# Optimization experiments

Measured on AMD Instinct MI355X. Metric: run time of the kernel, lower is better.

## Reference

```python
import jax, jax.numpy as jnp
import numpy as np

EPS = 1e-5  # torch LayerNorm default


def haar_dwt2(x):
    # pywt.dwt2(x, 'haar') on last two axes.
    # For each 2x2 block [[a,b],[c,d]]:
    #   LL=(a+b+c+d)/2, LH=(a+b-c-d)/2 (detail along rows),
    #   HL=(a-b+c-d)/2 (detail along cols), HH=(a-b-c+d)/2
    B, C, H, W = x.shape
    xb = x.reshape(B, C, H // 2, 2, W // 2, 2)
    a = xb[:, :, :, 0, :, 0]
    b = xb[:, :, :, 0, :, 1]
    c = xb[:, :, :, 1, :, 0]
    d = xb[:, :, :, 1, :, 1]
    ll = (a + b + c + d) * 0.5
    lh = (a + b - c - d) * 0.5
    hl = (a - b + c - d) * 0.5
    hh = (a - b - c + d) * 0.5
    return jnp.concatenate([ll, lh, hl, hh], axis=1)  # [B, 4C, H/2, W/2]


def setup_inputs() -> dict:
    key = jax.random.key(0)
    k1, k2 = jax.random.split(key)
    B, C, H, W = 16, 96, 256, 256
    x = jax.random.normal(k1, (B, C, H, W), dtype=jnp.float32)
    norm_w = jnp.ones((4 * C,), dtype=jnp.float32)
    norm_b = jnp.zeros((4 * C,), dtype=jnp.float32)
    w_red = jax.random.normal(k2, (4 * C, 2 * C), dtype=jnp.float32) * (1.0 / np.sqrt(4 * C))
    return {"x": x, "norm_w": norm_w, "norm_b": norm_b, "w_red": w_red}


def reference(x, norm_w, norm_b, w_red):
    B, C, H, W = x.shape
    y = haar_dwt2(x)                               # [B, 4C, H/2, W/2]
    y = y.reshape(B, 4 * C, -1).transpose(0, 2, 1)  # [B, L, 4C]
    mu = jnp.mean(y, axis=-1, keepdims=True)
    var = jnp.mean(jnp.square(y - mu), axis=-1, keepdims=True)
    y = (y - mu) * jax.lax.rsqrt(var + EPS) * norm_w + norm_b
    out = jnp.einsum('blc,cd->bld', y, w_red)       # [B, L, 2C]
    return out
```

## Files before the change

### kernel.cpp

```cpp
#include <hip/hip_runtime.h>
#include <hip/hip_bf16.h>

typedef __attribute__((ext_vector_type(8))) short short8;
typedef __attribute__((ext_vector_type(4))) float floatx4;

static __device__ __forceinline__ unsigned f2bf(float f) {
    unsigned u = __builtin_bit_cast(unsigned, f);
    unsigned r = u + 0x7fffu + ((u >> 16) & 1u);
    return r >> 16;
}
static __device__ __forceinline__ unsigned pk2bf(float lo, float hi) {
    return f2bf(lo) | (f2bf(hi) << 16);
}

__global__ __launch_bounds__(384)
void prep_kernel(const float* __restrict__ nw,
                 const float* __restrict__ nb,
                 const float* __restrict__ W,
                 __hip_bfloat16* __restrict__ Tt,
                 float* __restrict__ uvec,
                 float* __restrict__ vvec)
{
    __shared__ float su[384];
    __shared__ float sv[384];
    const int d = blockIdx.x;
    const int t = threadIdx.x;

    const int c  = t >> 2;
    const int rr = (t >> 1) & 1;
    const int q  = t & 1;

    float w0 = W[(0 * 96 + c) * 192 + d];
    float w1 = W[(1 * 96 + c) * 192 + d];
    float w2 = W[(2 * 96 + c) * 192 + d];
    float w3 = W[(3 * 96 + c) * 192 + d];
    float n0 = nw[0 * 96 + c];
    float n1 = nw[1 * 96 + c];
    float n2 = nw[2 * 96 + c];
    float n3 = nw[3 * 96 + c];

    float slh = rr ? -1.f : 1.f;
    float shl = q  ? -1.f : 1.f;
    float shh = (rr ^ q) ? -1.f : 1.f;
    float tv = 0.5f * (n0 * w0 + slh * n1 * w1 + shl * n2 * w2 + shh * n3 * w3);
    ((unsigned short*)Tt)[d * 384 + t] = (unsigned short)f2bf(tv);

    float wt = W[t * 192 + d];
    su[t] = nw[t] * wt;
    sv[t] = nb[t] * wt;
    __syncthreads();
    if (t < 64) {
        float a = su[t] + su[t + 64] + su[t + 128] + su[t + 192] + su[t + 256] + su[t + 320];
        float b = sv[t] + sv[t + 64] + sv[t + 128] + sv[t + 192] + sv[t + 256] + sv[t + 320];
        for (int off = 32; off; off >>= 1) {
            a += __shfl_down(a, off);
            b += __shfl_down(b, off);
        }
        if (t == 0) { uvec[d] = a; vvec[d] = b; }
    }
}

__global__ __launch_bounds__(256, 2)
void fused_kernel(const float* __restrict__ x,
                  const __hip_bfloat16* __restrict__ Tt,
                  const float* __restrict__ uvec,
                  const float* __restrict__ vvec,
                  float* __restrict__ out)
{
    constexpr int PK = 392;
    __shared__ __align__(16) __hip_bfloat16 As[64 * PK];
    __shared__ float S1p[256];
    __shared__ float S2p[256];
    __shared__ float2 ab[64];

    const int t  = threadIdx.x;
    const int bi = blockIdx.x;
    const int mb = bi & 1;
    const int h  = (bi >> 1) & 127;
    const int b  = bi >> 8;

    {
        const int m  = t & 63;
        const int cg = t >> 6;
        const float2* xrow =
            (const float2*)(x + ((size_t)b * 96 * 65536 + (size_t)(2 * h) * 256))
            + (mb * 64 + m);
        float s1 = 0.f, s2 = 0.f;
#pragma unroll
        for (int i = 0; i < 24; ++i) {
            const int ch = cg * 24 + i;
            const float2* p = xrow + (size_t)ch * 32768;
            float2 tp = p[0];
            float2 bt = p[128];
            s1 += tp.x;
            s2 += tp.x * tp.x + tp.y * tp.y + bt.x * bt.x + bt.y * bt.y;
            *(uint2*)(&As[m * PK + ch * 4]) =
                make_uint2(pk2bf(tp.x, tp.y), pk2bf(bt.x, bt.y));
        }
        S1p[t] = s1;
        S2p[t] = s2;
    }
    __syncthreads();
    if (t < 64) {
        float S1 = S1p[t] + S1p[t + 64] + S1p[t + 128] + S1p[t + 192];
        float S2 = S2p[t] + S2p[t + 64] + S2p[t + 128] + S2p[t + 192];
        float mu  = S1 * (2.0f / 384.0f);
        float var = S2 * (1.0f / 384.0f) - mu * mu;
        float rs  = rsqrtf(var + 1e-5f);
        ab[t] = make_float2(rs, -rs * mu);
    }
    __syncthreads();

    const int lane = t & 63;
    const int wv   = t >> 6;
    const int l15  = lane & 15;
    const int q2   = lane >> 4;

    const short8* Ap0 = (const short8*)(Tt + (size_t)(wv * 48 + l15) * 384 + q2 * 8);
    const short8* Bp0 = (const short8*)(&As[l15 * PK + q2 * 8]);

    floatx4 acc[3][4];
#pragma unroll
    for (int dt = 0; dt < 3; ++dt)
#pragma unroll
        for (int p = 0; p < 4; ++p)
            acc[dt][p] = (floatx4){0.f, 0.f, 0.f, 0.f};

#pragma unroll 2
    for (int ks = 0; ks < 12; ++ks) {
        short8 af[3], bf[4];
#pragma unroll
        for (int dt = 0; dt < 3; ++dt) af[dt] = Ap0[dt * 768 + ks * 4];
#pragma unroll
        for (int p = 0; p < 4; ++p) bf[p] = Bp0[p * 784 + ks * 4];
#pragma unroll
        for (int dt = 0; dt < 3; ++dt)
#pragma unroll
            for (int p = 0; p < 4; ++p)
                acc[dt][p] = __builtin_amdgcn_mfma_f32_16x16x32_bf16(
                    af[dt], bf[p], acc[dt][p], 0, 0, 0);
    }

    float2 abv[4];
#pragma unroll
    for (int p = 0; p < 4; ++p) abv[p] = ab[p * 16 + l15];

    const size_t outbase = ((size_t)b * 16384 + (size_t)h * 128 + mb * 64) * 192;
#pragma unroll
    for (int dt = 0; dt < 3; ++dt) {
        const int drow = wv * 48 + dt * 16 + q2 * 4;
        floatx4 uu = *(const floatx4*)(uvec + drow);
        floatx4 vv = *(const floatx4*)(vvec + drow);
#pragma unroll
        for (int p = 0; p < 4; ++p) {
            const int pos = p * 16 + l15;
            const float al = abv[p].x, be = abv[p].y;
            floatx4 o;
            o[0] = al * acc[dt][p][0] + be * uu[0] + vv[0];
            o[1] = al * acc[dt][p][1] + be * uu[1] + vv[1];
            o[2] = al * acc[dt][p][2] + be * uu[2] + vv[2];
            o[3] = al * acc[dt][p][3] + be * uu[3] + vv[3];
            *(floatx4*)(out + outbase + (size_t)pos * 192 + drow) = o;
        }
    }
}

extern "C" void kernel_launch(void* const* d_in, const int* in_sizes, int n_in,
                              void* d_out, int out_size, void* d_ws, size_t ws_size,
                              hipStream_t stream)
{
    const float* x  = (const float*)d_in[0];
    const float* nw = (const float*)d_in[1];
    const float* nb = (const float*)d_in[2];
    const float* W  = (const float*)d_in[3];
    float* out = (float*)d_out;

    __hip_bfloat16* Tt = (__hip_bfloat16*)d_ws;
    float* uvec = (float*)((char*)d_ws + 384 * 192 * 2);
    float* vvec = uvec + 192;

    prep_kernel<<<192, 384, 0, stream>>>(nw, nb, W, Tt, uvec, vvec);
    fused_kernel<<<4096, 256, 0, stream>>>(x, Tt, uvec, vvec, out);
}
```

Measured before the change: 634.5 us.

## Vectorize x loads with nontemporal float4, prefetch weights, raise occupancy

The load phase now reads x as 16-byte nontemporal vectors, with each thread covering two output positions across 12 channels instead of float2 loads over 24 channels. Partial sums are combined with a cross-lane shuffle before a smaller shared reduction. The first two k-steps of the weight tile and the u/v vectors are loaded before the x phase so their latency overlaps it. The bf16 packing uses the hardware cvt_pk instruction, and launch bounds ask for 3 blocks per CU. The risks are register pressure under the higher occupancy target and a different LDS store pattern that may cause bank conflicts.

```diff
diff --git a/kernel.cpp b/kernel.cpp
--- a/kernel.cpp
+++ b/kernel.cpp
@@ -10,7 +10,12 @@
     return r >> 16;
 }
 static __device__ __forceinline__ unsigned pk2bf(float lo, float hi) {
-    return f2bf(lo) | (f2bf(hi) << 16);
+    unsigned r;
+    asm("v_cvt_pk_bf16_f32 %0, %1, %2" : "=v"(r) : "v"(lo), "v"(hi));
+    return r;
+}
+static __device__ __forceinline__ floatx4 ntload(const floatx4* p) {
+    return __builtin_nontemporal_load(p);
 }
 
 __global__ __launch_bounds__(384)
@@ -60,7 +65,7 @@
     }
 }
 
-__global__ __launch_bounds__(256, 2)
+__global__ __launch_bounds__(256, 3)
 void fused_kernel(const float* __restrict__ x,
                   const __hip_bfloat16* __restrict__ Tt,
                   const float* __restrict__ uvec,
@@ -69,9 +74,7 @@
 {
     constexpr int PK = 392;
     __shared__ __align__(16) __hip_bfloat16 As[64 * PK];
-    __shared__ float S1p[256];
-    __shared__ float S2p[256];
-    __shared__ float2 ab[64];
+    __shared__ __align__(16) float S12[4][32][4];
 
     const int t  = threadIdx.x;
     const int bi = blockIdx.x;
@@ -79,44 +82,76 @@
     const int h  = (bi >> 1) & 127;
     const int b  = bi >> 8;
 
-    {
-        const int m  = t & 63;
-        const int cg = t >> 6;
-        const float2* xrow =
-            (const float2*)(x + ((size_t)b * 96 * 65536 + (size_t)(2 * h) * 256))
-            + (mb * 64 + m);
-        float s1 = 0.f, s2 = 0.f;
-#pragma unroll
-        for (int i = 0; i < 24; ++i) {
-            const int ch = cg * 24 + i;
-            const float2* p = xrow + (size_t)ch * 32768;
-            float2 tp = p[0];
-            float2 bt = p[128];
-            s1 += tp.x;
-            s2 += tp.x * tp.x + tp.y * tp.y + bt.x * bt.x + bt.y * bt.y;
-            *(uint2*)(&As[m * PK + ch * 4]) =
-                make_uint2(pk2bf(tp.x, tp.y), pk2bf(bt.x, bt.y));
-        }
-        S1p[t] = s1;
-        S2p[t] = s2;
-    }
-    __syncthreads();
-    if (t < 64) {
-        float S1 = S1p[t] + S1p[t + 64] + S1p[t + 128] + S1p[t + 192];
-        float S2 = S2p[t] + S2p[t + 64] + S2p[t + 128] + S2p[t + 192];
-        float mu  = S1 * (2.0f / 384.0f);
-        float var = S2 * (1.0f / 384.0f) - mu * mu;
-        float rs  = rsqrtf(var + 1e-5f);
-        ab[t] = make_float2(rs, -rs * mu);
-    }
-    __syncthreads();
-
     const int lane = t & 63;
     const int wv   = t >> 6;
     const int l15  = lane & 15;
     const int q2   = lane >> 4;
 
     const short8* Ap0 = (const short8*)(Tt + (size_t)(wv * 48 + l15) * 384 + q2 * 8);
+    short8 a0_0 = Ap0[0 * 768 + 0];
+    short8 a0_1 = Ap0[1 * 768 + 0];
+    short8 a0_2 = Ap0[2 * 768 + 0];
+    short8 a1_0 = Ap0[0 * 768 + 4];
+    short8 a1_1 = Ap0[1 * 768 + 4];
+    short8 a1_2 = Ap0[2 * 768 + 4];
+
+    {
+        const int f  = t & 31;
+        const int cg = t >> 5;
+        const floatx4* xt =
+            (const floatx4*)(x + ((size_t)b * 96 + cg) * 65536 + (size_t)(2 * h) * 256)
+            + (mb * 32 + f);
+        float s1a = 0.f, s2a = 0.f, s1b = 0.f, s2b = 0.f;
+#pragma unroll
+        for (int i = 0; i < 12; ++i) {
+            const floatx4* p = xt + (size_t)i * 131072;
+            floatx4 v = ntload(p);
+            floatx4 u = ntload(p + 64);
+            s1a += v[0];
+            s1b += v[2];
+            s2a += v[0] * v[0] + v[1] * v[1] + u[0] * u[0] + u[1] * u[1];
+            s2b += v[2] * v[2] + v[3] * v[3] + u[2] * u[2] + u[3] * u[3];
+            const int col = (cg + 8 * i) * 4;
+            *(uint2*)(&As[(2 * f) * PK + col]) =
+                make_uint2(pk2bf(v[0], v[1]), pk2bf(u[0], u[1]));
+            *(uint2*)(&As[(2 * f + 1) * PK + col]) =
+                make_uint2(pk2bf(v[2], v[3]), pk2bf(u[2], u[3]));
+        }
+        float r1a = s1a + __shfl_xor(s1a, 32);
+        float r2a = s2a + __shfl_xor(s2a, 32);
+        float r1b = s1b + __shfl_xor(s1b, 32);
+        float r2b = s2b + __shfl_xor(s2b, 32);
+        if (lane < 32) {
+            *(floatx4*)&S12[wv][f][0] = (floatx4){r1a, r2a, r1b, r2b};
+        }
+    }
+    __syncthreads();
+
+    if (t < 64) {
+        floatx4 r = *(const floatx4*)&S12[0][t >> 1][0];
+        r += *(const floatx4*)&S12[1][t >> 1][0];
+        r += *(const floatx4*)&S12[2][t >> 1][0];
+        r += *(const floatx4*)&S12[3][t >> 1][0];
+        float S1 = (t & 1) ? r[2] : r[0];
+        float S2 = (t & 1) ? r[3] : r[1];
+        float mu  = S1 * (2.0f / 384.0f);
+        float var = S2 * (1.0f / 384.0f) - mu * mu;
+        float rs  = rsqrtf(var + 1e-5f);
+        ((float2*)S12)[t] = make_float2(rs, -rs * mu);
+    }
+    __syncthreads();
+
+    const int dbase = wv * 48 + q2 * 4;
+    floatx4 uu[3], vv[3];
+#pragma unroll
+    for (int dt = 0; dt < 3; ++dt) {
+        uu[dt] = *(const floatx4*)(uvec + dbase + dt * 16);
+        vv[dt] = *(const floatx4*)(vvec + dbase + dt * 16);
+    }
+    float2 abv[4];
+#pragma unroll
+    for (int p = 0; p < 4; ++p) abv[p] = ((const float2*)S12)[p * 16 + l15];
+
     const short8* Bp0 = (const short8*)(&As[l15 * PK + q2 * 8]);
 
     floatx4 acc[3][4];
@@ -126,40 +161,55 @@
         for (int p = 0; p < 4; ++p)
             acc[dt][p] = (floatx4){0.f, 0.f, 0.f, 0.f};
 
-#pragma unroll 2
-    for (int ks = 0; ks < 12; ++ks) {
-        short8 af[3], bf[4];
-#pragma unroll
-        for (int dt = 0; dt < 3; ++dt) af[dt] = Ap0[dt * 768 + ks * 4];
-#pragma unroll
-        for (int p = 0; p < 4; ++p) bf[p] = Bp0[p * 784 + ks * 4];
+    {
+        short8 af[3] = {a0_0, a0_1, a0_2};
+        short8 bf[4];
+#pragma unroll
+        for (int p = 0; p < 4; ++p) bf[p] = Bp0[p * 784 + 0];
 #pragma unroll
         for (int dt = 0; dt < 3; ++dt)
 #pragma unroll
             for (int p = 0; p < 4; ++p)
                 acc[dt][p] = __builtin_amdgcn_mfma_f32_16x16x32_bf16(
                     af[dt], bf[p], acc[dt][p], 0, 0, 0);
-    }
-
-    float2 abv[4];
-#pragma unroll
-    for (int p = 0; p < 4; ++p) abv[p] = ab[p * 16 + l15];
+        short8 ag[3] = {a1_0, a1_1, a1_2};
+#pragma unroll
+        for (int p = 0; p < 4; ++p) bf[p] = Bp0[p * 784 + 4];
+#pragma unroll
+        for (int dt = 0; dt < 3; ++dt)
+#pragma unroll
+            for (int p = 0; p < 4; ++p)
+                acc[dt][p] = __builtin_amdgcn_mfma_f32_16x16x32_bf16(
+                    ag[dt], bf[p], acc[dt][p], 0, 0, 0);
+    }
+#pragma unroll 2
+    for (int ks = 2; ks < 12; ++ks) {
+        short8 af[3], bf[4];
+#pragma unroll
+        for (int dt = 0; dt < 3; ++dt) af[dt] = Ap0[dt * 768 + ks * 4];
+#pragma unroll
+        for (int p = 0; p < 4; ++p) bf[p] = Bp0[p * 784 + ks * 4];
+#pragma unroll
+        for (int dt = 0; dt < 3; ++dt)
+#pragma unroll
+            for (int p = 0; p < 4; ++p)
+                acc[dt][p] = __builtin_amdgcn_mfma_f32_16x16x32_bf16(
+                    af[dt], bf[p], acc[dt][p], 0, 0, 0);
+    }
 
     const size_t outbase = ((size_t)b * 16384 + (size_t)h * 128 + mb * 64) * 192;
 #pragma unroll
     for (int dt = 0; dt < 3; ++dt) {
         const int drow = wv * 48 + dt * 16 + q2 * 4;
-        floatx4 uu = *(const floatx4*)(uvec + drow);
-        floatx4 vv = *(const floatx4*)(vvec + drow);
 #pragma unroll
         for (int p = 0; p < 4; ++p) {
             const int pos = p * 16 + l15;
             const float al = abv[p].x, be = abv[p].y;
             floatx4 o;
-            o[0] = al * acc[dt][p][0] + be * uu[0] + vv[0];
-            o[1] = al * acc[dt][p][1] + be * uu[1] + vv[1];
-            o[2] = al * acc[dt][p][2] + be * uu[2] + vv[2];
-            o[3] = al * acc[dt][p][3] + be * uu[3] + vv[3];
+            o[0] = al * acc[dt][p][0] + be * uu[dt][0] + vv[dt][0];
+            o[1] = al * acc[dt][p][1] + be * uu[dt][1] + vv[dt][1];
+            o[2] = al * acc[dt][p][2] + be * uu[dt][2] + vv[dt][2];
+            o[3] = al * acc[dt][p][3] + be * uu[dt][3] + vv[dt][3];
             *(floatx4*)(out + outbase + (size_t)pos * 192 + drow) = o;
         }
     }
```

After: 610.3 us. 3.8% less time.
